# Optimization experiments

Measured on AMD Instinct MI355X. Metric: run time of the kernel, lower is better.

Reference implementation:

```python
import jax, jax.numpy as jnp
import numpy as np

N_NODES = 100000
N_EDGES = 1000000
N_GRAPHS = 64
NODE_IN = 4
HID = 64
SIG = 16
NEG_SLOPE = 0.2


def _gat_layer(x, src, dst, W, a_src, a_dst, bias, n_nodes, concat):
    # W: [H*D, F_in], a_src/a_dst: [H, D], bias: [H*D] or [D]
    H, D = a_src.shape
    h = (x @ W.T).reshape(-1, H, D)                      # [N, H, D]
    alpha_src = jnp.sum(h * a_src[None], axis=-1)        # [N, H]
    alpha_dst = jnp.sum(h * a_dst[None], axis=-1)        # [N, H]
    e = alpha_src[src] + alpha_dst[dst]                  # [E, H]
    e = jax.nn.leaky_relu(e, NEG_SLOPE)
    # segment softmax over edges grouped by destination node
    e_max = jax.ops.segment_max(e, dst, num_segments=n_nodes)   # [N, H]
    e_exp = jnp.exp(e - e_max[dst])                              # [E, H]
    denom = jax.ops.segment_sum(e_exp, dst, num_segments=n_nodes)
    alpha = e_exp / denom[dst]                                   # [E, H]
    out = jax.ops.segment_sum(alpha[:, :, None] * h[src], dst, num_segments=n_nodes)  # [N,H,D]
    if concat:
        out = out.reshape(-1, H * D)
    else:
        out = out.mean(axis=1)
    return out + bias


def setup_inputs() -> dict:
    key = jax.random.key(0)
    ks = jax.random.split(key, 16)
    x = jax.random.normal(ks[0], (N_NODES, NODE_IN), dtype=jnp.float32)
    edge_index = jax.random.randint(ks[1], (2, N_EDGES), 0, N_NODES, dtype=jnp.int32)
    batch = jnp.sort(jax.random.randint(ks[2], (N_NODES,), 0, N_GRAPHS, dtype=jnp.int32))
    s = 0.1
    # conv1: heads=2, concat -> out 128
    w1 = jax.random.normal(ks[3], (2 * HID, NODE_IN), dtype=jnp.float32) * s
    att_src1 = jax.random.normal(ks[4], (2, HID), dtype=jnp.float32) * s
    att_dst1 = jax.random.normal(ks[5], (2, HID), dtype=jnp.float32) * s
    b1 = jnp.zeros((2 * HID,), dtype=jnp.float32)
    # conv2: heads=1, mean -> out 64
    w2 = jax.random.normal(ks[6], (HID, 2 * HID), dtype=jnp.float32) * s
    att_src2 = jax.random.normal(ks[7], (1, HID), dtype=jnp.float32) * s
    att_dst2 = jax.random.normal(ks[8], (1, HID), dtype=jnp.float32) * s
    b2 = jnp.zeros((HID,), dtype=jnp.float32)
    wp = jax.random.normal(ks[9], (SIG, HID), dtype=jnp.float32) * s
    bp = jnp.zeros((SIG,), dtype=jnp.float32)
    return {"x": x, "edge_index": edge_index, "batch": batch,
            "w1": w1, "att_src1": att_src1, "att_dst1": att_dst1, "b1": b1,
            "w2": w2, "att_src2": att_src2, "att_dst2": att_dst2, "b2": b2,
            "wp": wp, "bp": bp}


def reference(x, edge_index, batch, w1, att_src1, att_dst1, b1,
              w2, att_src2, att_dst2, b2, wp, bp):
    n = x.shape[0]
    loops = jnp.arange(n, dtype=edge_index.dtype)
    src = jnp.concatenate([edge_index[0], loops])  # PyG GATConv adds self-loops
    dst = jnp.concatenate([edge_index[1], loops])
    h = jax.nn.elu(_gat_layer(x, src, dst, w1, att_src1, att_dst1, b1, n, concat=True))
    h = jax.nn.elu(_gat_layer(h, src, dst, w2, att_src2, att_dst2, b2, n, concat=False))
    # global mean pool by graph id
    sums = jax.ops.segment_sum(h, batch, num_segments=N_GRAPHS)
    cnts = jax.ops.segment_sum(jnp.ones((n,), h.dtype), batch, num_segments=N_GRAPHS)
    pooled = sums / jnp.maximum(cnts, 1.0)[:, None]
    return (pooled @ wp.T + bp).squeeze()
```

## Files before the change

kernel.cpp:

```cpp
#include <hip/hip_runtime.h>
#include <hip/hip_fp16.h>

#define N_NODES  100000
#define N_EDGES  1000000
#define E_TOT    1100000
#define E_CAP    1900000
#define N_GRAPHS 64

typedef _Float16 half8 __attribute__((ext_vector_type(8)));
typedef float    f32x4 __attribute__((ext_vector_type(4)));

__device__ __forceinline__ float elu_f(float v) {
    return v > 0.f ? v : expm1f(v);
}

__device__ __forceinline__ float lrelu(float v) {
    return v > 0.f ? v : 0.2f * v;
}

__global__ void k_preall(const float* __restrict__ w1,
                         const float* __restrict__ as1v, const float* __restrict__ ad1v,
                         const float* __restrict__ w2,
                         const float* __restrict__ as2v, const float* __restrict__ ad2v,
                         float* __restrict__ A1, float* __restrict__ D1,
                         float* __restrict__ B2, float* __restrict__ E2,
                         __half* __restrict__ w2frag)
{
    if (blockIdx.x == 0) {
        int t = threadIdx.x;
        if (t < 128) {
            float acc = 0.f;
            for (int d = 0; d < 64; ++d) acc += w2[d * 128 + t] * as2v[d];
            B2[t] = acc;
        } else {
            int k = t - 128;
            float acc = 0.f;
            for (int d = 0; d < 64; ++d) acc += w2[d * 128 + k] * ad2v[d];
            E2[k] = acc;
        }
        if (t < 8) {
            int h = t >> 2, k = t & 3;
            float acc = 0.f;
            for (int d = 0; d < 64; ++d) acc += w1[(h * 64 + d) * 4 + k] * as1v[h * 64 + d];
            A1[t] = acc;
        } else if (t < 16) {
            int i = t - 8, h = i >> 2, k = i & 3;
            float acc = 0.f;
            for (int d = 0; d < 64; ++d) acc += w1[(h * 64 + d) * 4 + k] * ad1v[h * 64 + d];
            D1[i] = acc;
        }
    } else {
        int f = (blockIdx.x - 1) * 256 + threadIdx.x;
        int j = f & 7, ln = (f >> 3) & 63, g = f >> 9;
        int nt = g >> 2, ks = g & 3;
        int col = nt * 16 + (ln & 15);
        int k   = ks * 32 + ((ln >> 4) << 3) + j;
        w2frag[f] = __float2half(w2[col * 128 + k]);
    }
}

__global__ void k_count(const int* __restrict__ ei, int* __restrict__ deg, int* __restrict__ pos)
{
    int e = blockIdx.x * blockDim.x + threadIdx.x;
    if (e >= E_TOT) return;
    int dst = (e < N_EDGES) ? ei[N_EDGES + e] : (e - N_EDGES);
    pos[e] = atomicAdd(&deg[dst], 1);
}

__global__ void k_scan1(const int* __restrict__ deg, int* __restrict__ rowptr, int* __restrict__ bsum)
{
    __shared__ int sh[256];
    int tid = threadIdx.x;
    int i = blockIdx.x * 256 + tid;
    int v = (i <= N_NODES) ? ((deg[i] + 7) & ~7) : 0;
    int acc = v;
    sh[tid] = acc; __syncthreads();
    for (int off = 1; off < 256; off <<= 1) {
        int add = (tid >= off) ? sh[tid - off] : 0;
        __syncthreads();
        acc += add;
        sh[tid] = acc;
        __syncthreads();
    }
    if (i <= N_NODES) rowptr[i] = acc - v;
    if (tid == 255) bsum[blockIdx.x] = acc;
}

__global__ void k_scan2(int* __restrict__ bsum, int nb)
{
    __shared__ int sh[512];
    int tid = threadIdx.x;
    int v = (tid < nb) ? bsum[tid] : 0;
    int acc = v;
    sh[tid] = acc; __syncthreads();
    for (int off = 1; off < 512; off <<= 1) {
        int add = (tid >= off) ? sh[tid - off] : 0;
        __syncthreads();
        acc += add;
        sh[tid] = acc;
        __syncthreads();
    }
    if (tid < nb) bsum[tid] = acc - v;
}

__global__ void k_scan3(int* __restrict__ rowptr, const int* __restrict__ bsum)
{
    int i = blockIdx.x * 256 + threadIdx.x;
    if (i <= N_NODES) rowptr[i] += bsum[blockIdx.x];
}

__global__ void k_scatter(const int* __restrict__ ei, const int* __restrict__ rowptr,
                          const int* __restrict__ pos, int* __restrict__ srcs)
{
    int e = blockIdx.x * blockDim.x + threadIdx.x;
    if (e >= E_TOT) return;
    int src = (e < N_EDGES) ? ei[e] : (e - N_EDGES);
    int dst = (e < N_EDGES) ? ei[N_EDGES + e] : (e - N_EDGES);
    srcs[rowptr[dst] + pos[e]] = src;
}

__global__ void __launch_bounds__(256) k_gather1x(
    const int* __restrict__ srcs, const int* __restrict__ rowptr, const int* __restrict__ deg,
    const float* __restrict__ x,
    const float* __restrict__ A1c, const float* __restrict__ D1c,
    float4* __restrict__ agg0, float4* __restrict__ agg1, float2* __restrict__ wsA)
{
    const int tid  = threadIdx.x;
    const int n    = blockIdx.x * 16 + (tid >> 4);
    const int lane = tid & 15;
    if (n >= N_NODES) return;

    const float4 A0 = ((const float4*)A1c)[0], A1v = ((const float4*)A1c)[1];
    const float4 D0 = ((const float4*)D1c)[0], D1v = ((const float4*)D1c)[1];
    const float4 xn = ((const float4*)x)[n];
    const float ad0 = xn.x * D0.x + xn.y * D0.y + xn.z * D0.z + xn.w * D0.w;
    const float ad1 = xn.x * D1v.x + xn.y * D1v.y + xn.z * D1v.z + xn.w * D1v.w;

    const int beg = rowptr[n], rend = beg + deg[n];
    float4 acc0 = {0.f, 0.f, 0.f, 0.f}, acc1 = {0.f, 0.f, 0.f, 0.f};
    float ws0 = 0.f, ws1 = 0.f;
    for (int j = beg + lane; j < rend; j += 16) {
        const int s = srcs[j];
        const float4 xs = ((const float4*)x)[s];
        const float as0 = xs.x * A0.x + xs.y * A0.y + xs.z * A0.z + xs.w * A0.w;
        const float as1 = xs.x * A1v.x + xs.y * A1v.y + xs.z * A1v.z + xs.w * A1v.w;
        const float w0 = __expf(lrelu(as0 + ad0));
        const float w1 = __expf(lrelu(as1 + ad1));
        acc0.x = fmaf(w0, xs.x, acc0.x); acc0.y = fmaf(w0, xs.y, acc0.y);
        acc0.z = fmaf(w0, xs.z, acc0.z); acc0.w = fmaf(w0, xs.w, acc0.w);
        acc1.x = fmaf(w1, xs.x, acc1.x); acc1.y = fmaf(w1, xs.y, acc1.y);
        acc1.z = fmaf(w1, xs.z, acc1.z); acc1.w = fmaf(w1, xs.w, acc1.w);
        ws0 += w0; ws1 += w1;
    }
    #pragma unroll
    for (int off = 1; off < 16; off <<= 1) {
        acc0.x += __shfl_xor(acc0.x, off, 64);
        acc0.y += __shfl_xor(acc0.y, off, 64);
        acc0.z += __shfl_xor(acc0.z, off, 64);
        acc0.w += __shfl_xor(acc0.w, off, 64);
        acc1.x += __shfl_xor(acc1.x, off, 64);
        acc1.y += __shfl_xor(acc1.y, off, 64);
        acc1.z += __shfl_xor(acc1.z, off, 64);
        acc1.w += __shfl_xor(acc1.w, off, 64);
        ws0    += __shfl_xor(ws0,    off, 64);
        ws1    += __shfl_xor(ws1,    off, 64);
    }
    if (lane == 0) {
        agg0[n] = acc0;
        agg1[n] = acc1;
        wsA[n]  = make_float2(ws0, ws1);
    }
}

#define H2_NPB 64
#define SROW_H_LD 136
__global__ void __launch_bounds__(256) k_h2f(
    const float4* __restrict__ agg0, const float4* __restrict__ agg1,
    const float2* __restrict__ wsA,
    const float* __restrict__ w1, const float* __restrict__ b1,
    const __half* __restrict__ w2frag,
    const float* __restrict__ B2, const float* __restrict__ E2,
    __half* __restrict__ h2h, float* __restrict__ as2, float* __restrict__ ad2)
{
    __shared__ __align__(16) _Float16 srow[H2_NPB * SROW_H_LD];
    const int tid = threadIdx.x;
    const int bn  = blockIdx.x * H2_NPB;

    #pragma unroll 4
    for (int t = 0; t < 16; ++t) {
        int i = tid + t * 256;
        int r = i >> 6, c2 = i & 63;
        int n = bn + r;
        int head = c2 >> 5;
        float4 a; float ws;
        if (n < N_NODES) {
            a = head ? agg1[n] : agg0[n];
            float2 w = wsA[n];
            ws = head ? w.y : w.x;
        } else { a = make_float4(0.f, 0.f, 0.f, 0.f); ws = 1.f; }
        const float4 wA = ((const float4*)w1)[2 * c2];
        const float4 wB = ((const float4*)w1)[2 * c2 + 1];
        const float2 bb = ((const float2*)b1)[c2];
        float inv = 1.f / ws;
        float v0 = elu_f((a.x * wA.x + a.y * wA.y + a.z * wA.z + a.w * wA.w) * inv + bb.x);
        float v1 = elu_f((a.x * wB.x + a.y * wB.y + a.z * wB.z + a.w * wB.w) * inv + bb.y);
        *(__half2*)&srow[r * SROW_H_LD + 2 * c2] = __floats2half2_rn(v0, v1);
    }
    __syncthreads();

    {
        int r = tid >> 2, q = tid & 3;
        const __half2* row = (const __half2*)&srow[r * SROW_H_LD];
        float ps = 0.f, pd = 0.f;
        #pragma unroll 4
        for (int i = 0; i < 16; ++i) {
            int c2 = q * 16 + i;
            float2 v  = __half22float2(row[c2]);
            float2 Bv = ((const float2*)B2)[c2];
            float2 Ev = ((const float2*)E2)[c2];
            ps += v.x * Bv.x + v.y * Bv.y;
            pd += v.x * Ev.x + v.y * Ev.y;
        }
        ps += __shfl_xor(ps, 1, 64); ps += __shfl_xor(ps, 2, 64);
        pd += __shfl_xor(pd, 1, 64); pd += __shfl_xor(pd, 2, 64);
        int n = bn + r;
        if (q == 0 && n < N_NODES) { as2[n] = ps; ad2[n] = pd; }
    }

    const int lane = tid & 63;
    const int wv   = tid >> 6;
    const int mrow = lane & 15;
    const int kc   = lane >> 4;
    f32x4 acc[4] = {{0.f,0.f,0.f,0.f},{0.f,0.f,0.f,0.f},{0.f,0.f,0.f,0.f},{0.f,0.f,0.f,0.f}};
    const half8* __restrict__ wf = (const half8*)w2frag;
    #pragma unroll
    for (int ks = 0; ks < 4; ++ks) {
        const half8 af = *(const half8*)&srow[(wv * 16 + mrow) * SROW_H_LD + ks * 32 + kc * 8];
        #pragma unroll
        for (int nt = 0; nt < 4; ++nt) {
            const half8 bf = wf[(nt * 4 + ks) * 64 + lane];
            acc[nt] = __builtin_amdgcn_mfma_f32_16x16x32_f16(af, bf, acc[nt], 0, 0, 0);
        }
    }
    #pragma unroll
    for (int nt = 0; nt < 4; ++nt) {
        #pragma unroll
        for (int reg = 0; reg < 4; ++reg) {
            int node = bn + wv * 16 + ((lane >> 4) << 2) + reg;
            int dim  = nt * 16 + (lane & 15);
            if (node < N_NODES) h2h[(size_t)node * 64 + dim] = __float2half(acc[nt][reg]);
        }
    }
}

__global__ void __launch_bounds__(256) k_weights2(
    const int* __restrict__ rowptr, const int* __restrict__ deg, int* __restrict__ srcs,
    const float* __restrict__ as2, const float* __restrict__ ad2,
    float* __restrict__ w0p)
{
    int n = blockIdx.x * 16 + (threadIdx.x >> 4);
    int lane = threadIdx.x & 15;
    if (n >= N_NODES) return;
    int beg = rowptr[n], pend = rowptr[n + 1], rend = beg + deg[n];
    float adv = ad2[n];
    for (int j = beg + lane; j < pend; j += 16) {
        if (j < rend) {
            w0p[j] = __expf(lrelu(as2[srcs[j]] + adv));
        } else {
            srcs[j] = 0;
            w0p[j] = 0.f;
        }
    }
}

__global__ void __launch_bounds__(256) k_gather2(
    const int* __restrict__ srcs, const int* __restrict__ rowptr,
    const float* __restrict__ wcsr, const _Float16* __restrict__ h2h,
    const float* __restrict__ b2, float* __restrict__ out2, int nbase)
{
    const int tid  = threadIdx.x;
    const int n    = nbase + blockIdx.x * 4 + (tid >> 6);
    const int lane = tid & 63;
    const int eg   = lane >> 3;
    const int dq   = lane & 7;
    const int beg = rowptr[n], end = rowptr[n + 1];

    half8 hacc = {0, 0, 0, 0, 0, 0, 0, 0};
    float wsum = 0.f;
    for (int j = beg + eg; j < end; j += 8) {
        const int   s = srcs[j];
        const float w = wcsr[j];
        const half8 v = *(const half8*)&h2h[(size_t)s * 64 + dq * 8];
        const _Float16 wh = (_Float16)w;
        const half8 ws8 = {wh, wh, wh, wh, wh, wh, wh, wh};
        hacc += v * ws8;
        wsum += w;
    }
    float a0 = (float)hacc[0], a1 = (float)hacc[1], a2 = (float)hacc[2], a3 = (float)hacc[3];
    float a4 = (float)hacc[4], a5 = (float)hacc[5], a6 = (float)hacc[6], a7 = (float)hacc[7];
    #pragma unroll
    for (int off = 8; off < 64; off <<= 1) {
        a0 += __shfl_xor(a0, off, 64);
        a1 += __shfl_xor(a1, off, 64);
        a2 += __shfl_xor(a2, off, 64);
        a3 += __shfl_xor(a3, off, 64);
        a4 += __shfl_xor(a4, off, 64);
        a5 += __shfl_xor(a5, off, 64);
        a6 += __shfl_xor(a6, off, 64);
        a7 += __shfl_xor(a7, off, 64);
        wsum += __shfl_xor(wsum, off, 64);
    }
    if (eg == 0) {
        const float inv = 1.f / wsum;
        const float4 bA = ((const float4*)b2)[dq * 2];
        const float4 bB = ((const float4*)b2)[dq * 2 + 1];
        float4 oA, oB;
        oA.x = elu_f(a0 * inv + bA.x);
        oA.y = elu_f(a1 * inv + bA.y);
        oA.z = elu_f(a2 * inv + bA.z);
        oA.w = elu_f(a3 * inv + bA.w);
        oB.x = elu_f(a4 * inv + bB.x);
        oB.y = elu_f(a5 * inv + bB.y);
        oB.z = elu_f(a6 * inv + bB.z);
        oB.w = elu_f(a7 * inv + bB.w);
        float4* orow = (float4*)(out2 + (size_t)n * 64);
        orow[dq * 2]     = oA;
        orow[dq * 2 + 1] = oB;
    }
}

__global__ void __launch_bounds__(256) k_pool(
    const float* __restrict__ out2, const int* __restrict__ batch,
    float* __restrict__ pool, float* __restrict__ cnt)
{
    const int wv = threadIdx.x >> 6, d = threadIdx.x & 63;
    const int wid = blockIdx.x * 4 + wv;
    const int per = (N_NODES + 2047) / 2048;
    int n0 = wid * per, n1 = min(n0 + per, N_NODES);
    if (n0 >= n1) return;
    float acc = 0.f; int g = batch[n0]; int run = 0;
    for (int n = n0; n < n1; ++n) {
        int gn = batch[n];
        if (gn != g) {
            atomicAdd(&pool[g * 64 + d], acc);
            if (d == 0) atomicAdd(&cnt[g], (float)run);
            acc = 0.f; run = 0; g = gn;
        }
        acc += out2[(size_t)n * 64 + d];
        ++run;
    }
    atomicAdd(&pool[g * 64 + d], acc);
    if (d == 0) atomicAdd(&cnt[g], (float)run);
}

__global__ void k_head(const float* __restrict__ pool, const float* __restrict__ cnt,
                       const float* __restrict__ wp, const float* __restrict__ bp,
                       float* __restrict__ out)
{
    int t = threadIdx.x;
    int g = t >> 4, s = t & 15;
    float c = cnt[g]; if (c < 1.f) c = 1.f;
    float acc = bp[s];
    for (int d = 0; d < 64; ++d) acc += (pool[g * 64 + d] / c) * wp[s * 64 + d];
    out[g * 16 + s] = acc;
}

extern "C" void kernel_launch(void* const* d_in, const int* in_sizes, int n_in,
                              void* d_out, int out_size, void* d_ws, size_t ws_size,
                              hipStream_t stream)
{
    const float* x     = (const float*)d_in[0];
    const int*   ei    = (const int*)  d_in[1];
    const int*   batch = (const int*)  d_in[2];
    const float* w1    = (const float*)d_in[3];
    const float* asr1  = (const float*)d_in[4];
    const float* adr1  = (const float*)d_in[5];
    const float* b1    = (const float*)d_in[6];
    const float* w2    = (const float*)d_in[7];
    const float* asr2  = (const float*)d_in[8];
    const float* adr2  = (const float*)d_in[9];
    const float* b2    = (const float*)d_in[10];
    const float* wp    = (const float*)d_in[11];
    const float* bp    = (const float*)d_in[12];
    float* out = (float*)d_out;

    float4* agg0 = (float4*)d_ws;
    float4* agg1 = agg0 + N_NODES;
    float2* wsA  = (float2*)(agg1 + N_NODES);
    __half* h2h  = (__half*)(wsA + N_NODES);
    float* out2  = (float*)(h2h + (size_t)N_NODES * 64);
    float* as2   = out2 + (size_t)N_NODES * 64;
    float* ad2   = as2 + N_NODES;
    float* pool  = ad2 + N_NODES;
    float* cnt   = pool + N_GRAPHS * 64;
    int* deg     = (int*)(cnt + N_GRAPHS);
    int* rowptr  = deg + N_NODES + 1;
    int* pos     = rowptr + N_NODES + 1;
    int* srcs    = pos + E_TOT;
    float* wcsr  = (float*)(srcs + E_CAP);
    int* bsum    = (int*)(wcsr + E_CAP);
    float* A1    = (float*)(bsum + 512);
    float* D1    = A1 + 8;
    float* B2    = D1 + 8;
    float* E2    = B2 + 128;
    __half* w2frag = (__half*)(((uintptr_t)(E2 + 128) + 15) & ~(uintptr_t)15);

    hipMemsetAsync(deg, 0, (size_t)(N_NODES + 1) * sizeof(int), stream);
    hipMemsetAsync(pool, 0, (size_t)(N_GRAPHS * 64 + N_GRAPHS) * sizeof(float), stream);

    k_preall<<<33, 256, 0, stream>>>(w1, asr1, adr1, w2, asr2, adr2, A1, D1, B2, E2, w2frag);

    const int eb  = (E_TOT + 255) / 256;
    const int nb1 = (N_NODES + 1 + 255) / 256;
    k_count<<<eb, 256, 0, stream>>>(ei, deg, pos);
    k_scan1<<<nb1, 256, 0, stream>>>(deg, rowptr, bsum);
    k_scan2<<<1, 512, 0, stream>>>(bsum, nb1);
    k_scan3<<<nb1, 256, 0, stream>>>(rowptr, bsum);
    k_scatter<<<eb, 256, 0, stream>>>(ei, rowptr, pos, srcs);

    const int gb = (N_NODES + 15) / 16;
    k_gather1x<<<gb, 256, 0, stream>>>(srcs, rowptr, deg, x, A1, D1, agg0, agg1, wsA);

    k_h2f<<<(N_NODES + H2_NPB - 1) / H2_NPB, 256, 0, stream>>>(
        agg0, agg1, wsA, w1, b1, w2frag, B2, E2, h2h, as2, ad2);

    k_weights2<<<gb, 256, 0, stream>>>(rowptr, deg, srcs, as2, ad2, wcsr);
    k_gather2<<<N_NODES / 8, 256, 0, stream>>>(srcs, rowptr, wcsr, (const _Float16*)h2h,
                                               b2, out2, 0);
    k_gather2<<<N_NODES / 8, 256, 0, stream>>>(srcs, rowptr, wcsr, (const _Float16*)h2h,
                                               b2, out2, N_NODES / 2);

    k_pool<<<512, 256, 0, stream>>>(out2, batch, pool, cnt);
    k_head<<<1, 1024, 0, stream>>>(pool, cnt, wp, bp, out);
}
```

Baseline: 234.2 us.

## Build CSR via two-level bucket sort with shared-memory atomics

Replaces the global-atomic degree count, three-kernel scan and random scatter with a two-pass bucket sort. Edges are first binned into 512-node buckets using per-block shared-memory histograms and packed src/local-dst words. Each bucket is then processed by one block that computes degrees, padded row pointers and final positions using shared-memory atomics. The aim is to remove heavily contended global atomics and scattered global writes, at the cost of more kernel launches and an extra pass over the edge list.

New measurement: 215.0 us. 1.09x faster.

```diff
diff --git a/kernel.cpp b/kernel.cpp
--- a/kernel.cpp
+++ b/kernel.cpp
@@ -6,6 +6,12 @@
 #define E_TOT    1100000
 #define E_CAP    1900000
 #define N_GRAPHS 64
+
+#define BSH    9
+#define BSIZE  512
+#define NBUCK  ((N_NODES + BSIZE - 1) / BSIZE)
+#define CHUNK  4096
+#define NBLKS  ((E_TOT + CHUNK - 1) / CHUNK)
 
 typedef _Float16 half8 __attribute__((ext_vector_type(8)));
 typedef float    f32x4 __attribute__((ext_vector_type(4)));
@@ -59,64 +65,139 @@
     }
 }
 
-__global__ void k_count(const int* __restrict__ ei, int* __restrict__ deg, int* __restrict__ pos)
-{
-    int e = blockIdx.x * blockDim.x + threadIdx.x;
-    if (e >= E_TOT) return;
-    int dst = (e < N_EDGES) ? ei[N_EDGES + e] : (e - N_EDGES);
-    pos[e] = atomicAdd(&deg[dst], 1);
-}
-
-__global__ void k_scan1(const int* __restrict__ deg, int* __restrict__ rowptr, int* __restrict__ bsum)
+__global__ void __launch_bounds__(256) k_bin1(
+    const int* __restrict__ ei, int* __restrict__ bucketCount, int* __restrict__ blockoff)
+{
+    __shared__ int hist[NBUCK];
+    const int t = threadIdx.x;
+    for (int i = t; i < NBUCK; i += 256) hist[i] = 0;
+    __syncthreads();
+    const int e0 = blockIdx.x * CHUNK;
+    for (int i = t; i < CHUNK; i += 256) {
+        int e = e0 + i;
+        if (e < E_TOT) {
+            int dst = (e < N_EDGES) ? ei[N_EDGES + e] : (e - N_EDGES);
+            atomicAdd(&hist[dst >> BSH], 1);
+        }
+    }
+    __syncthreads();
+    for (int i = t; i < NBUCK; i += 256)
+        blockoff[blockIdx.x * NBUCK + i] = atomicAdd(&bucketCount[i], hist[i]);
+}
+
+__global__ void k_bscan(const int* __restrict__ bucketCount, int* __restrict__ bucketStart)
 {
     __shared__ int sh[256];
-    int tid = threadIdx.x;
-    int i = blockIdx.x * 256 + tid;
-    int v = (i <= N_NODES) ? ((deg[i] + 7) & ~7) : 0;
+    int t = threadIdx.x;
+    int v = (t < NBUCK) ? bucketCount[t] : 0;
     int acc = v;
-    sh[tid] = acc; __syncthreads();
+    sh[t] = acc; __syncthreads();
     for (int off = 1; off < 256; off <<= 1) {
-        int add = (tid >= off) ? sh[tid - off] : 0;
+        int add = (t >= off) ? sh[t - off] : 0;
         __syncthreads();
-        acc += add;
-        sh[tid] = acc;
+        acc += add; sh[t] = acc; __syncthreads();
+    }
+    if (t < NBUCK) bucketStart[t] = acc - v;
+}
+
+__global__ void __launch_bounds__(256) k_bin2(
+    const int* __restrict__ ei, const int* __restrict__ bucketStart,
+    const int* __restrict__ blockoff, unsigned int* __restrict__ bucketed)
+{
+    __shared__ int cur[NBUCK];
+    const int t = threadIdx.x;
+    for (int i = t; i < NBUCK; i += 256)
+        cur[i] = bucketStart[i] + blockoff[blockIdx.x * NBUCK + i];
+    __syncthreads();
+    const int e0 = blockIdx.x * CHUNK;
+    for (int i = t; i < CHUNK; i += 256) {
+        int e = e0 + i;
+        if (e < E_TOT) {
+            int src = (e < N_EDGES) ? ei[e] : (e - N_EDGES);
+            int dst = (e < N_EDGES) ? ei[N_EDGES + e] : (e - N_EDGES);
+            int b = dst >> BSH;
+            int p = atomicAdd(&cur[b], 1);
+            bucketed[p] = (unsigned)src | ((unsigned)(dst & (BSIZE - 1)) << 17);
+        }
+    }
+}
+
+__global__ void __launch_bounds__(256) k_bhist(
+    const unsigned int* __restrict__ bucketed,
+    const int* __restrict__ bucketStart, const int* __restrict__ bucketCount,
+    int* __restrict__ deg, int* __restrict__ rowptr, int* __restrict__ bucketPad)
+{
+    __shared__ int hist[BSIZE];
+    __shared__ int sh[256];
+    const int t = threadIdx.x;
+    const int b = blockIdx.x;
+    hist[t] = 0; hist[t + 256] = 0;
+    __syncthreads();
+    const int beg = bucketStart[b], cnt = bucketCount[b];
+    for (int i = t; i < cnt; i += 256)
+        atomicAdd(&hist[bucketed[beg + i] >> 17], 1);
+    __syncthreads();
+    int h0 = hist[2 * t], h1 = hist[2 * t + 1];
+    int a = (h0 + 7) & ~7, c = (h1 + 7) & ~7;
+    int s = a + c;
+    sh[t] = s; __syncthreads();
+    for (int off = 1; off < 256; off <<= 1) {
+        int add = (t >= off) ? sh[t - off] : 0;
         __syncthreads();
-    }
-    if (i <= N_NODES) rowptr[i] = acc - v;
-    if (tid == 255) bsum[blockIdx.x] = acc;
-}
-
-__global__ void k_scan2(int* __restrict__ bsum, int nb)
-{
-    __shared__ int sh[512];
-    int tid = threadIdx.x;
-    int v = (tid < nb) ? bsum[tid] : 0;
+        s += add; sh[t] = s; __syncthreads();
+    }
+    int base = s - a - c;
+    const int n0 = b * BSIZE;
+    int na = n0 + 2 * t, nb = n0 + 2 * t + 1;
+    if (na < N_NODES) { deg[na] = h0; rowptr[na] = base; }
+    if (nb < N_NODES) { deg[nb] = h1; rowptr[nb] = base + a; }
+    if (t == 255) bucketPad[b] = s;
+}
+
+__global__ void k_bscan2(const int* __restrict__ bucketPad, int* __restrict__ bucketBase,
+                         int* __restrict__ rowptr)
+{
+    __shared__ int sh[256];
+    int t = threadIdx.x;
+    int v = (t < NBUCK) ? bucketPad[t] : 0;
     int acc = v;
-    sh[tid] = acc; __syncthreads();
-    for (int off = 1; off < 512; off <<= 1) {
-        int add = (tid >= off) ? sh[tid - off] : 0;
+    sh[t] = acc; __syncthreads();
+    for (int off = 1; off < 256; off <<= 1) {
+        int add = (t >= off) ? sh[t - off] : 0;
         __syncthreads();
-        acc += add;
-        sh[tid] = acc;
-        __syncthreads();
-    }
-    if (tid < nb) bsum[tid] = acc - v;
-}
-
-__global__ void k_scan3(int* __restrict__ rowptr, const int* __restrict__ bsum)
-{
-    int i = blockIdx.x * 256 + threadIdx.x;
-    if (i <= N_NODES) rowptr[i] += bsum[blockIdx.x];
-}
-
-__global__ void k_scatter(const int* __restrict__ ei, const int* __restrict__ rowptr,
-                          const int* __restrict__ pos, int* __restrict__ srcs)
-{
-    int e = blockIdx.x * blockDim.x + threadIdx.x;
-    if (e >= E_TOT) return;
-    int src = (e < N_EDGES) ? ei[e] : (e - N_EDGES);
-    int dst = (e < N_EDGES) ? ei[N_EDGES + e] : (e - N_EDGES);
-    srcs[rowptr[dst] + pos[e]] = src;
+        acc += add; sh[t] = acc; __syncthreads();
+    }
+    if (t < NBUCK) bucketBase[t] = acc - v;
+    if (t == NBUCK - 1) rowptr[N_NODES] = acc;
+}
+
+__global__ void __launch_bounds__(256) k_bscat(
+    const unsigned int* __restrict__ bucketed,
+    const int* __restrict__ bucketStart, const int* __restrict__ bucketCount,
+    const int* __restrict__ bucketBase, int* __restrict__ rowptr, int* __restrict__ srcs)
+{
+    __shared__ int cur[BSIZE];
+    const int t = threadIdx.x;
+    const int b = blockIdx.x;
+    const int base = bucketBase[b];
+    const int n0 = b * BSIZE;
+    #pragma unroll
+    for (int k = 0; k < 2; ++k) {
+        int nl = t + k * 256;
+        int n = n0 + nl;
+        if (n < N_NODES) {
+            int r = rowptr[n] + base;
+            rowptr[n] = r;
+            cur[nl] = r;
+        }
+    }
+    __syncthreads();
+    const int beg = bucketStart[b], cnt = bucketCount[b];
+    for (int i = t; i < cnt; i += 256) {
+        unsigned p = bucketed[beg + i];
+        int rank = atomicAdd(&cur[p >> 17], 1);
+        srcs[rank] = (int)(p & 0x1FFFFu);
+    }
 }
 
 __global__ void __launch_bounds__(256) k_gather1x(
@@ -394,29 +475,32 @@
     float* pool  = ad2 + N_NODES;
     float* cnt   = pool + N_GRAPHS * 64;
     int* deg     = (int*)(cnt + N_GRAPHS);
-    int* rowptr  = deg + N_NODES + 1;
-    int* pos     = rowptr + N_NODES + 1;
-    int* srcs    = pos + E_TOT;
+    int* rowptr  = deg + N_NODES;
+    unsigned int* bucketed = (unsigned int*)(rowptr + N_NODES + 1);
+    int* srcs    = (int*)(bucketed + E_TOT);
     float* wcsr  = (float*)(srcs + E_CAP);
-    int* bsum    = (int*)(wcsr + E_CAP);
-    float* A1    = (float*)(bsum + 512);
+    int* blockoff    = (int*)(wcsr + E_CAP);
+    int* bucketCount = blockoff + NBLKS * NBUCK;
+    int* bucketStart = bucketCount + NBUCK;
+    int* bucketPad   = bucketStart + NBUCK;
+    int* bucketBase  = bucketPad + NBUCK;
+    float* A1    = (float*)(bucketBase + NBUCK);
     float* D1    = A1 + 8;
     float* B2    = D1 + 8;
     float* E2    = B2 + 128;
     __half* w2frag = (__half*)(((uintptr_t)(E2 + 128) + 15) & ~(uintptr_t)15);
 
-    hipMemsetAsync(deg, 0, (size_t)(N_NODES + 1) * sizeof(int), stream);
+    hipMemsetAsync(bucketCount, 0, NBUCK * sizeof(int), stream);
     hipMemsetAsync(pool, 0, (size_t)(N_GRAPHS * 64 + N_GRAPHS) * sizeof(float), stream);
 
     k_preall<<<33, 256, 0, stream>>>(w1, asr1, adr1, w2, asr2, adr2, A1, D1, B2, E2, w2frag);
 
-    const int eb  = (E_TOT + 255) / 256;
-    const int nb1 = (N_NODES + 1 + 255) / 256;
-    k_count<<<eb, 256, 0, stream>>>(ei, deg, pos);
-    k_scan1<<<nb1, 256, 0, stream>>>(deg, rowptr, bsum);
-    k_scan2<<<1, 512, 0, stream>>>(bsum, nb1);
-    k_scan3<<<nb1, 256, 0, stream>>>(rowptr, bsum);
-    k_scatter<<<eb, 256, 0, stream>>>(ei, rowptr, pos, srcs);
+    k_bin1 <<<NBLKS, 256, 0, stream>>>(ei, bucketCount, blockoff);
+    k_bscan<<<1, 256, 0, stream>>>(bucketCount, bucketStart);
+    k_bin2 <<<NBLKS, 256, 0, stream>>>(ei, bucketStart, blockoff, bucketed);
+    k_bhist<<<NBUCK, 256, 0, stream>>>(bucketed, bucketStart, bucketCount, deg, rowptr, bucketPad);
+    k_bscan2<<<1, 256, 0, stream>>>(bucketPad, bucketBase, rowptr);
+    k_bscat<<<NBUCK, 256, 0, stream>>>(bucketed, bucketStart, bucketCount, bucketBase, rowptr, srcs);
 
     const int gb = (N_NODES + 15) / 16;
     k_gather1x<<<gb, 256, 0, stream>>>(srcs, rowptr, deg, x, A1, D1, agg0, agg1, wsA);
```
